# Optimization experiments

Hardware: AMD Instinct MI355X
Metric: run time of the kernel (lower is better)

Reference implementation:

```python
import jax, jax.numpy as jnp
import numpy as np

N, E, D, L, G, C = 20000, 320000, 512, 6, 64, 10
EPS = 1e-5


def setup_inputs() -> dict:
    key = jax.random.key(0)
    ks = jax.random.split(key, 8)
    s = 0.05  # small init scale to keep activations sane across 6 layers
    x = jax.random.normal(ks[0], (N, D), jnp.float32)
    edge_index = jax.random.randint(ks[1], (2, E), 0, N, jnp.int32)
    batch = jnp.sort(jax.random.randint(ks[2], (N,), 0, G, jnp.int32))
    W_rel = jax.random.normal(ks[3], (L, D, D), jnp.float32) * s
    b_rel = jnp.zeros((L, D), jnp.float32)
    W_root = jax.random.normal(ks[4], (L, D, D), jnp.float32) * s
    gamma = jnp.ones((L, D), jnp.float32)
    beta = jnp.zeros((L, D), jnp.float32)
    lin_w = jax.random.normal(ks[5], (D, C), jnp.float32) * s
    lin_b = jnp.zeros((C,), jnp.float32)
    return {"x": x, "edge_index": edge_index, "batch": batch,
            "W_rel": W_rel, "b_rel": b_rel, "W_root": W_root,
            "gamma": gamma, "beta": beta, "lin_w": lin_w, "lin_b": lin_b}


def reference(x, edge_index, batch, W_rel, b_rel, W_root, gamma, beta, lin_w, lin_b):
    # PyG GraphConv (aggr='add'): out = segment_sum(x[src] -> dst) @ W_rel + b_rel + x @ W_root
    src, dst = edge_index[0], edge_index[1]
    n = x.shape[0]
    for l in range(W_rel.shape[0]):  # 6 structurally identical layers
        agg = jax.ops.segment_sum(x[src], dst, num_segments=n)  # [N, D]
        h = agg @ W_rel[l] + b_rel[l] + x @ W_root[l]
        # BatchNorm1d in training mode: biased batch statistics over nodes
        mu = jnp.mean(h, axis=0)
        var = jnp.mean(jnp.square(h - mu), axis=0)
        x = jax.nn.relu((h - mu) * jax.lax.rsqrt(var + EPS) * gamma[l] + beta[l])
    # global_mean_pool over per-node graph ids
    sums = jax.ops.segment_sum(x, batch, num_segments=G)              # [G, D]
    counts = jax.ops.segment_sum(jnp.ones((n,), x.dtype), batch, num_segments=G)
    pooled = sums / jnp.maximum(counts, 1.0)[:, None]
    return pooled @ lin_w + lin_b  # [G, C]
```

## Files before the change

kernel.cpp:

```cpp
#include <hip/hip_runtime.h>


typedef unsigned short u16;
typedef unsigned int u32;
typedef __attribute__((ext_vector_type(8))) short bf16x8;
typedef __attribute__((ext_vector_type(4))) float f32x4;

#define DFEAT 512
#define KDIM 1024
#define NLAYER 6
#define NGRAPH 64
#define NCLS 10
#define BN_EPS 1e-5f

__device__ __forceinline__ float bf_lo(u32 u) { union { u32 i; float f; } v; v.i = u << 16; return v.f; }
__device__ __forceinline__ float bf_hi(u32 u) { union { u32 i; float f; } v; v.i = u & 0xFFFF0000u; return v.f; }
__device__ __forceinline__ u16 f2bf(float f) {
  union { float f; u32 i; } v; v.f = f;
  u32 r = v.i + 0x7FFFu + ((v.i >> 16) & 1u);
  return (u16)(r >> 16);
}
__device__ __forceinline__ u32 pack2(float lo, float hi) {
  return (u32)f2bf(lo) | ((u32)f2bf(hi) << 16);
}

__device__ __forceinline__ void gload_lds16(const u16* g, u16* lds_base) {
  __builtin_amdgcn_global_load_lds(
      (const __attribute__((address_space(1))) u32*)g,
      (__attribute__((address_space(3))) u32*)lds_base, 16, 0, 0);
}

__global__ void hist_kernel(const int* __restrict__ ei, int* __restrict__ counts, int E) {
  int e = blockIdx.x * 256 + threadIdx.x;
  if (e < E) atomicAdd(&counts[ei[E + e]], 1);
}

__global__ __launch_bounds__(1024) void scan_kernel(const int* __restrict__ counts,
                                                    int* __restrict__ row_ptr, int n) {
  __shared__ int buf[1024];
  int tid = threadIdx.x;
  int carry = 0;
  for (int base = 0; base < n; base += 1024) {
    int i = base + tid;
    int v = (i < n) ? counts[i] : 0;
    buf[tid] = v;
    __syncthreads();
    int x = v;
    for (int off = 1; off < 1024; off <<= 1) {
      int t = (tid >= off) ? buf[tid - off] : 0;
      __syncthreads();
      x += t;
      buf[tid] = x;
      __syncthreads();
    }
    if (i < n) row_ptr[i] = carry + x - v;
    int tot = buf[1023];
    __syncthreads();
    carry += tot;
  }
  if (tid == 0) row_ptr[n] = carry;
}

__global__ void scatter_kernel(const int* __restrict__ ei, int* __restrict__ cursor,
                               int* __restrict__ csr_src, int E) {
  int e = blockIdx.x * 256 + threadIdx.x;
  if (e < E) {
    int d = ei[E + e];
    int pos = atomicAdd(&cursor[d], 1);
    csr_src[pos] = ei[e];
  }
}

__global__ void wconv_kernel(const float* __restrict__ Wrel, const float* __restrict__ Wroot,
                             u16* __restrict__ Wt) {
  int idx = blockIdx.x * 256 + threadIdx.x;
  int k = idx & 1023;
  int n = (idx >> 10) & 511;
  int l = idx >> 19;
  float v = (k < DFEAT) ? Wrel[((size_t)l * DFEAT + k) * DFEAT + n]
                        : Wroot[((size_t)l * DFEAT + (k - DFEAT)) * DFEAT + n];
  Wt[idx] = f2bf(v);
}

__global__ void xconv_kernel(const float* __restrict__ x, u16* __restrict__ A, int M) {
  int idx = blockIdx.x * 256 + threadIdx.x;
  int row = idx >> 7;
  int c4 = (idx & 127) * 4;
  if (row >= M) return;
  float4 v = *(const float4*)&x[(size_t)row * DFEAT + c4];
  uint2 o; o.x = pack2(v.x, v.y); o.y = pack2(v.z, v.w);
  *(uint2*)&A[(size_t)row * KDIM + DFEAT + c4] = o;
}

__device__ __forceinline__ void add8(uint4 v, float* a) {
  a[0] += bf_lo(v.x); a[1] += bf_hi(v.x);
  a[2] += bf_lo(v.y); a[3] += bf_hi(v.y);
  a[4] += bf_lo(v.z); a[5] += bf_hi(v.z);
  a[6] += bf_lo(v.w); a[7] += bf_hi(v.w);
}

__global__ __launch_bounds__(256) void gather_kernel(u16* __restrict__ A,
                                                     const int* __restrict__ row_ptr,
                                                     const int* __restrict__ csr_src, int n) {
  int b = blockIdx.x;
  int slice = b & 7;
  int grp = b >> 3;
  int wid = threadIdx.x >> 6, lane = threadIdx.x & 63;
  int dsub = lane >> 3, fl = lane & 7;
  int dst = grp * 32 + wid * 8 + dsub;
  if (dst >= n) return;
  int cc = slice * 64 + fl * 8;
  const u16* Sx = A + DFEAT;
  int beg = row_ptr[dst], end = row_ptr[dst + 1];
  float a[8] = {};
  int e = beg;
  for (; e + 3 < end; e += 4) {
    int s0 = csr_src[e], s1 = csr_src[e + 1], s2 = csr_src[e + 2], s3 = csr_src[e + 3];
    uint4 v0 = *(const uint4*)&Sx[(size_t)s0 * KDIM + cc];
    uint4 v1 = *(const uint4*)&Sx[(size_t)s1 * KDIM + cc];
    uint4 v2 = *(const uint4*)&Sx[(size_t)s2 * KDIM + cc];
    uint4 v3 = *(const uint4*)&Sx[(size_t)s3 * KDIM + cc];
    add8(v0, a); add8(v1, a); add8(v2, a); add8(v3, a);
  }
  for (; e < end; ++e) {
    int s = csr_src[e];
    uint4 v = *(const uint4*)&Sx[(size_t)s * KDIM + cc];
    add8(v, a);
  }
  uint4 o;
  o.x = pack2(a[0], a[1]); o.y = pack2(a[2], a[3]);
  o.z = pack2(a[4], a[5]); o.w = pack2(a[6], a[7]);
  *(uint4*)&A[(size_t)dst * KDIM + cc] = o;
}

#define BM 128
#define BN 128
#define BK 64
__global__ __launch_bounds__(256, 2) void gemm_kernel(const u16* __restrict__ A,
                                                      const u16* __restrict__ Bt,
                                                      const float* __restrict__ bias,
                                                      u16* __restrict__ Hb,
                                                      float* __restrict__ sums, int M) {
  const int lin = blockIdx.x;
  const int bx = ((lin >> 5) << 3) + (lin & 7);
  const int by = (lin >> 3) & 3;
  const int m0 = bx * BM;
  if (m0 >= M) return;
  const int n0 = by * BN;

  __shared__ u16 As[BM * BK];
  __shared__ u16 Bs[BN * BK];
  __shared__ float sred[2 * BN];
  const int tid = threadIdx.x;
  const int wid = tid >> 6, lane = tid & 63;
  const int wm = wid >> 1, wn = wid & 1;
  const int l16 = lane & 15, quad = lane >> 4;

  if (tid < 2 * BN) sred[tid] = 0.f;

  const int dr = lane >> 3;
  const int gcol = ((lane & 7) ^ dr) * 8;
  int arow[4], brow[4];
#pragma unroll
  for (int t = 0; t < 4; t++) {
    int r = wid * 32 + t * 8 + dr;
    int ar = m0 + r; if (ar >= M) ar = M - 1;
    arow[t] = ar;
    brow[t] = n0 + r;
  }

  f32x4 acc[4][4] = {};

  for (int k0 = 0; k0 < KDIM; k0 += BK) {
    __syncthreads();
#pragma unroll
    for (int t = 0; t < 4; t++)
      gload_lds16(&A[(size_t)arow[t] * KDIM + k0 + gcol], &As[(wid * 32 + t * 8) * BK]);
#pragma unroll
    for (int t = 0; t < 4; t++)
      gload_lds16(&Bt[(size_t)brow[t] * KDIM + k0 + gcol], &Bs[(wid * 32 + t * 8) * BK]);
    __syncthreads();
    bf16x8 af[2][4], bfr[2][4];
#pragma unroll
    for (int h = 0; h < 2; h++) {
      int slot = ((h * 4 + quad) ^ (l16 & 7)) * 8;
#pragma unroll
      for (int i = 0; i < 4; i++) {
        af[h][i]  = *(const bf16x8*)&As[(wm * 64 + i * 16 + l16) * BK + slot];
        bfr[h][i] = *(const bf16x8*)&Bs[(wn * 64 + i * 16 + l16) * BK + slot];
      }
    }
#pragma unroll
    for (int h = 0; h < 2; h++)
#pragma unroll
      for (int i = 0; i < 4; i++)
#pragma unroll
        for (int j = 0; j < 4; j++)
          acc[i][j] = __builtin_amdgcn_mfma_f32_16x16x32_bf16(af[h][i], bfr[h][j], acc[i][j], 0, 0, 0);
  }

#pragma unroll
  for (int j = 0; j < 4; j++) {
    int col = n0 + wn * 64 + j * 16 + l16;
    float bv = bias[col];
    float s = 0.f, s2 = 0.f;
#pragma unroll
    for (int i = 0; i < 4; i++) {
      int rbase = m0 + wm * 64 + i * 16 + quad * 4;
#pragma unroll
      for (int r = 0; r < 4; r++) {
        int row = rbase + r;
        if (row < M) {
          float v = acc[i][j][r] + bv;
          Hb[(size_t)row * DFEAT + col] = f2bf(v);
          s += v; s2 += v * v;
        }
      }
    }
    s  += __shfl_xor(s, 16);  s  += __shfl_xor(s, 32);
    s2 += __shfl_xor(s2, 16); s2 += __shfl_xor(s2, 32);
    if (quad == 0) {
      int cl = wn * 64 + j * 16 + l16;
      atomicAdd(&sred[cl], s);
      atomicAdd(&sred[BN + cl], s2);
    }
  }
  __syncthreads();
  if (tid < BN) {
    atomicAdd(&sums[n0 + tid], sred[tid]);
    atomicAdd(&sums[DFEAT + n0 + tid], sred[BN + tid]);
  }
}

__global__ void norm_kernel(const u16* __restrict__ Hb, const float* __restrict__ sums,
                            const float* __restrict__ gamma, const float* __restrict__ beta,
                            u16* __restrict__ A, int M, float invN) {
  int idx = blockIdx.x * 256 + threadIdx.x;
  int row = idx >> 7;
  int c4 = (idx & 127) * 4;
  if (row >= M) return;
  float sc[4], sh[4];
#pragma unroll
  for (int j = 0; j < 4; j++) {
    int c = c4 + j;
    float mu = sums[c] * invN;
    float var = sums[DFEAT + c] * invN - mu * mu;
    float s = gamma[c] * rsqrtf(var + BN_EPS);
    sc[j] = s;
    sh[j] = beta[c] - mu * s;
  }
  uint2 h = *(const uint2*)&Hb[(size_t)row * DFEAT + c4];
  float x0 = fmaxf(bf_lo(h.x) * sc[0] + sh[0], 0.f);
  float x1 = fmaxf(bf_hi(h.x) * sc[1] + sh[1], 0.f);
  float x2 = fmaxf(bf_lo(h.y) * sc[2] + sh[2], 0.f);
  float x3 = fmaxf(bf_hi(h.y) * sc[3] + sh[3], 0.f);
  uint2 o; o.x = pack2(x0, x1); o.y = pack2(x2, x3);
  *(uint2*)&A[(size_t)row * KDIM + DFEAT + c4] = o;
}

__device__ __forceinline__ int lower_bound_dev(const int* a, int n, int v) {
  int lo = 0, hi = n;
  while (lo < hi) { int mid = (lo + hi) >> 1; if (a[mid] < v) lo = mid + 1; else hi = mid; }
  return lo;
}

__global__ __launch_bounds__(1024) void pool_kernel(const u16* __restrict__ Hb,
                                                    const float* __restrict__ sums,
                                                    const float* __restrict__ gamma,
                                                    const float* __restrict__ beta,
                                                    const int* __restrict__ batch,
                                                    float* __restrict__ pooled, int n, float invN) {
  __shared__ float red[DFEAT];
  int g = blockIdx.x;
  int tid = threadIdx.x;
  if (tid < DFEAT) red[tid] = 0.f;
  int lo = lower_bound_dev(batch, n, g);
  int hi = lower_bound_dev(batch, n, g + 1);
  int rowOff = tid >> 6, lane = tid & 63;
  int c0 = lane * 8;
  float sc[8], sh[8];
#pragma unroll
  for (int j = 0; j < 8; j++) {
    int c = c0 + j;
    float mu = sums[c] * invN;
    float var = sums[DFEAT + c] * invN - mu * mu;
    float s = gamma[c] * rsqrtf(var + BN_EPS);
    sc[j] = s;
    sh[j] = beta[c] - mu * s;
  }
  float a[8] = {};
  for (int r = lo + rowOff; r < hi; r += 16) {
    uint4 v = *(const uint4*)&Hb[(size_t)r * DFEAT + c0];
    float e0 = bf_lo(v.x), e1 = bf_hi(v.x), e2 = bf_lo(v.y), e3 = bf_hi(v.y);
    float e4 = bf_lo(v.z), e5 = bf_hi(v.z), e6 = bf_lo(v.w), e7 = bf_hi(v.w);
    a[0] += fmaxf(e0 * sc[0] + sh[0], 0.f); a[1] += fmaxf(e1 * sc[1] + sh[1], 0.f);
    a[2] += fmaxf(e2 * sc[2] + sh[2], 0.f); a[3] += fmaxf(e3 * sc[3] + sh[3], 0.f);
    a[4] += fmaxf(e4 * sc[4] + sh[4], 0.f); a[5] += fmaxf(e5 * sc[5] + sh[5], 0.f);
    a[6] += fmaxf(e6 * sc[6] + sh[6], 0.f); a[7] += fmaxf(e7 * sc[7] + sh[7], 0.f);
  }
  __syncthreads();
#pragma unroll
  for (int j = 0; j < 8; j++) atomicAdd(&red[c0 + j], a[j]);
  __syncthreads();
  if (tid < DFEAT) pooled[g * DFEAT + tid] = red[tid] / fmaxf((float)(hi - lo), 1.0f);
}

__global__ __launch_bounds__(64) void final_kernel(const float* __restrict__ pooled,
                                                   const float* __restrict__ lin_w,
                                                   const float* __restrict__ lin_b,
                                                   float* __restrict__ out) {
  int g = blockIdx.x;
  int lane = threadIdx.x;
  float acc[NCLS] = {};
  float4 p0 = *(const float4*)&pooled[g * DFEAT + lane * 8];
  float4 p1 = *(const float4*)&pooled[g * DFEAT + lane * 8 + 4];
  float pv[8] = {p0.x, p0.y, p0.z, p0.w, p1.x, p1.y, p1.z, p1.w};
#pragma unroll
  for (int j = 0; j < 8; j++) {
    int k = lane * 8 + j;
#pragma unroll
    for (int c = 0; c < NCLS; c++) acc[c] += pv[j] * lin_w[k * NCLS + c];
  }
#pragma unroll
  for (int off = 32; off > 0; off >>= 1)
#pragma unroll
    for (int c = 0; c < NCLS; c++) acc[c] += __shfl_down(acc[c], off);
  if (lane == 0)
#pragma unroll
    for (int c = 0; c < NCLS; c++) out[g * NCLS + c] = acc[c] + lin_b[c];
}

extern "C" void kernel_launch(void* const* d_in, const int* in_sizes, int n_in,
                              void* d_out, int out_size, void* d_ws, size_t ws_size,
                              hipStream_t stream) {
  const float* x      = (const float*)d_in[0];
  const int*   ei     = (const int*)d_in[1];
  const int*   batch  = (const int*)d_in[2];
  const float* W_rel  = (const float*)d_in[3];
  const float* b_rel  = (const float*)d_in[4];
  const float* W_root = (const float*)d_in[5];
  const float* gamma  = (const float*)d_in[6];
  const float* beta   = (const float*)d_in[7];
  const float* lin_w  = (const float*)d_in[8];
  const float* lin_b  = (const float*)d_in[9];
  float* out = (float*)d_out;

  const int N = in_sizes[0] / DFEAT;
  const int E = in_sizes[1] / 2;

  char* p = (char*)d_ws;
  u16*   A       = (u16*)p;    p += (size_t)N * KDIM * 2;
  u16*   Hb      = (u16*)p;    p += (size_t)N * DFEAT * 2;
  u16*   Wt      = (u16*)p;    p += (size_t)NLAYER * DFEAT * KDIM * 2;
  int*   row_ptr = (int*)p;    p += ((size_t)(N + 1) * 4 + 15) / 16 * 16;
  int*   cursor  = (int*)p;    p += (size_t)N * 4;
  int*   csr_src = (int*)p;    p += (size_t)E * 4;
  float* sums    = (float*)p;  p += (size_t)NLAYER * 2 * DFEAT * 4;
  float* pooled  = (float*)p;  p += (size_t)NGRAPH * DFEAT * 4;

  hipMemsetAsync(cursor, 0, (size_t)N * 4, stream);
  hipMemsetAsync(sums, 0, (size_t)NLAYER * 2 * DFEAT * 4, stream);

  hist_kernel<<<(E + 255) / 256, 256, 0, stream>>>(ei, cursor, E);
  scan_kernel<<<1, 1024, 0, stream>>>(cursor, row_ptr, N);
  hipMemcpyAsync(cursor, row_ptr, (size_t)N * 4, hipMemcpyDeviceToDevice, stream);
  scatter_kernel<<<(E + 255) / 256, 256, 0, stream>>>(ei, cursor, csr_src, E);

  wconv_kernel<<<(NLAYER * DFEAT * KDIM) / 256, 256, 0, stream>>>(W_rel, W_root, Wt);
  xconv_kernel<<<(N * 128 + 255) / 256, 256, 0, stream>>>(x, A, N);

  const int ngrp = (N + 31) / 32;
  const int gather_grid = ngrp * 8;
  const int gemm_rows = (N + BM - 1) / BM;
  const int gemm_grid = ((gemm_rows + 7) / 8) * 8 * 4;

  for (int l = 0; l < NLAYER; ++l) {
    float* sums_l = sums + (size_t)l * 2 * DFEAT;
    gather_kernel<<<gather_grid, 256, 0, stream>>>(A, row_ptr, csr_src, N);
    gemm_kernel<<<gemm_grid, 256, 0, stream>>>(A, Wt + (size_t)l * DFEAT * KDIM,
                                               b_rel + (size_t)l * DFEAT, Hb, sums_l, N);
    if (l < NLAYER - 1)
      norm_kernel<<<(N * 128 + 255) / 256, 256, 0, stream>>>(
          Hb, sums_l, gamma + (size_t)l * DFEAT, beta + (size_t)l * DFEAT, A, N, 1.0f / (float)N);
  }

  pool_kernel<<<NGRAPH, 1024, 0, stream>>>(Hb, sums + (size_t)(NLAYER - 1) * 2 * DFEAT,
                                           gamma + (size_t)(NLAYER - 1) * DFEAT,
                                           beta + (size_t)(NLAYER - 1) * DFEAT,
                                           batch, pooled, N, 1.0f / (float)N);
  final_kernel<<<NGRAPH, 64, 0, stream>>>(pooled, lin_w, lin_b, out);
}
```

Measured before the change: 653.9 us.

## Fuse BatchNorm+ReLU into neighbor gather and stage GEMM output through LDS

Drops the separate norm kernel. The next layer's gather now reads the raw bf16 GEMM output Hb, applies BatchNorm scale/shift and ReLU per gathered neighbor, and also writes the normalized self row into the root half of A. The GEMM epilogue writes its tile into shared memory first and then does coalesced 16-byte row stores to Hb, where before it did scattered 2-byte stores. Fusing saves one full read/write pass per layer. In exchange, the gather recomputes the affine+ReLU for each edge, and the GEMM epilogue gains an extra sync and a larger shared buffer.

```diff
diff --git a/kernel.cpp b/kernel.cpp
--- a/kernel.cpp
+++ b/kernel.cpp
@@ -92,14 +92,12 @@
   *(uint2*)&A[(size_t)row * KDIM + DFEAT + c4] = o;
 }
 
-__device__ __forceinline__ void add8(uint4 v, float* a) {
-  a[0] += bf_lo(v.x); a[1] += bf_hi(v.x);
-  a[2] += bf_lo(v.y); a[3] += bf_hi(v.y);
-  a[4] += bf_lo(v.z); a[5] += bf_hi(v.z);
-  a[6] += bf_lo(v.w); a[7] += bf_hi(v.w);
-}
-
 __global__ __launch_bounds__(256) void gather_kernel(u16* __restrict__ A,
+                                                     const u16* __restrict__ S, int sstride,
+                                                     const float* __restrict__ sums,
+                                                     const float* __restrict__ gamma,
+                                                     const float* __restrict__ beta,
+                                                     float invN,
                                                      const int* __restrict__ row_ptr,
                                                      const int* __restrict__ csr_src, int n) {
   int b = blockIdx.x;
@@ -110,32 +108,71 @@
   int dst = grp * 32 + wid * 8 + dsub;
   if (dst >= n) return;
   int cc = slice * 64 + fl * 8;
-  const u16* Sx = A + DFEAT;
+  const bool aff = (sums != nullptr);
+  float sc[8], sh[8];
+#pragma unroll
+  for (int j = 0; j < 8; j++) {
+    if (aff) {
+      int c = cc + j;
+      float mu = sums[c] * invN;
+      float var = sums[DFEAT + c] * invN - mu * mu;
+      float s = gamma[c] * rsqrtf(var + BN_EPS);
+      sc[j] = s;
+      sh[j] = beta[c] - mu * s;
+    } else { sc[j] = 1.f; sh[j] = 0.f; }
+  }
+
+#define AFF8(v, a)                                                          \
+  {                                                                         \
+    float e0 = bf_lo(v.x), e1 = bf_hi(v.x), e2 = bf_lo(v.y), e3 = bf_hi(v.y); \
+    float e4 = bf_lo(v.z), e5 = bf_hi(v.z), e6 = bf_lo(v.w), e7 = bf_hi(v.w); \
+    if (aff) {                                                              \
+      a[0] += fmaxf(e0 * sc[0] + sh[0], 0.f); a[1] += fmaxf(e1 * sc[1] + sh[1], 0.f); \
+      a[2] += fmaxf(e2 * sc[2] + sh[2], 0.f); a[3] += fmaxf(e3 * sc[3] + sh[3], 0.f); \
+      a[4] += fmaxf(e4 * sc[4] + sh[4], 0.f); a[5] += fmaxf(e5 * sc[5] + sh[5], 0.f); \
+      a[6] += fmaxf(e6 * sc[6] + sh[6], 0.f); a[7] += fmaxf(e7 * sc[7] + sh[7], 0.f); \
+    } else {                                                                \
+      a[0] += e0; a[1] += e1; a[2] += e2; a[3] += e3;                       \
+      a[4] += e4; a[5] += e5; a[6] += e6; a[7] += e7;                       \
+    }                                                                       \
+  }
+
   int beg = row_ptr[dst], end = row_ptr[dst + 1];
   float a[8] = {};
   int e = beg;
   for (; e + 3 < end; e += 4) {
     int s0 = csr_src[e], s1 = csr_src[e + 1], s2 = csr_src[e + 2], s3 = csr_src[e + 3];
-    uint4 v0 = *(const uint4*)&Sx[(size_t)s0 * KDIM + cc];
-    uint4 v1 = *(const uint4*)&Sx[(size_t)s1 * KDIM + cc];
-    uint4 v2 = *(const uint4*)&Sx[(size_t)s2 * KDIM + cc];
-    uint4 v3 = *(const uint4*)&Sx[(size_t)s3 * KDIM + cc];
-    add8(v0, a); add8(v1, a); add8(v2, a); add8(v3, a);
+    uint4 v0 = *(const uint4*)&S[(size_t)s0 * sstride + cc];
+    uint4 v1 = *(const uint4*)&S[(size_t)s1 * sstride + cc];
+    uint4 v2 = *(const uint4*)&S[(size_t)s2 * sstride + cc];
+    uint4 v3 = *(const uint4*)&S[(size_t)s3 * sstride + cc];
+    AFF8(v0, a); AFF8(v1, a); AFF8(v2, a); AFF8(v3, a);
   }
   for (; e < end; ++e) {
     int s = csr_src[e];
-    uint4 v = *(const uint4*)&Sx[(size_t)s * KDIM + cc];
-    add8(v, a);
+    uint4 v = *(const uint4*)&S[(size_t)s * sstride + cc];
+    AFF8(v, a);
   }
   uint4 o;
   o.x = pack2(a[0], a[1]); o.y = pack2(a[2], a[3]);
   o.z = pack2(a[4], a[5]); o.w = pack2(a[6], a[7]);
   *(uint4*)&A[(size_t)dst * KDIM + cc] = o;
+
+  if (aff) {
+    uint4 vd = *(const uint4*)&S[(size_t)dst * sstride + cc];
+    float xd[8] = {};
+    AFF8(vd, xd);
+    uint4 ox; ox.x = pack2(xd[0], xd[1]); ox.y = pack2(xd[2], xd[3]);
+    ox.z = pack2(xd[4], xd[5]); ox.w = pack2(xd[6], xd[7]);
+    *(uint4*)&A[(size_t)dst * KDIM + DFEAT + cc] = ox;
+  }
+#undef AFF8
 }
 
 #define BM 128
 #define BN 128
 #define BK 64
+#define CSTR 132
 __global__ __launch_bounds__(256, 2) void gemm_kernel(const u16* __restrict__ A,
                                                       const u16* __restrict__ Bt,
                                                       const float* __restrict__ bias,
@@ -148,9 +185,10 @@
   if (m0 >= M) return;
   const int n0 = by * BN;
 
-  __shared__ u16 As[BM * BK];
-  __shared__ u16 Bs[BN * BK];
+  __shared__ u16 smem[BM * CSTR];
   __shared__ float sred[2 * BN];
+  u16* As = smem;
+  u16* Bs = smem + BM * BK;
   const int tid = threadIdx.x;
   const int wid = tid >> 6, lane = tid & 63;
   const int wm = wid >> 1, wn = wid & 1;
@@ -199,63 +237,48 @@
           acc[i][j] = __builtin_amdgcn_mfma_f32_16x16x32_bf16(af[h][i], bfr[h][j], acc[i][j], 0, 0, 0);
   }
 
+  __syncthreads();
+
 #pragma unroll
   for (int j = 0; j < 4; j++) {
-    int col = n0 + wn * 64 + j * 16 + l16;
-    float bv = bias[col];
+    int colt = wn * 64 + j * 16 + l16;
+    float bv = bias[n0 + colt];
     float s = 0.f, s2 = 0.f;
 #pragma unroll
     for (int i = 0; i < 4; i++) {
-      int rbase = m0 + wm * 64 + i * 16 + quad * 4;
+      int rbase = wm * 64 + i * 16 + quad * 4;
 #pragma unroll
       for (int r = 0; r < 4; r++) {
-        int row = rbase + r;
-        if (row < M) {
-          float v = acc[i][j][r] + bv;
-          Hb[(size_t)row * DFEAT + col] = f2bf(v);
-          s += v; s2 += v * v;
-        }
+        int rowt = rbase + r;
+        float v = acc[i][j][r] + bv;
+        smem[rowt * CSTR + colt] = f2bf(v);
+        if (m0 + rowt < M) { s += v; s2 += v * v; }
       }
     }
     s  += __shfl_xor(s, 16);  s  += __shfl_xor(s, 32);
     s2 += __shfl_xor(s2, 16); s2 += __shfl_xor(s2, 32);
     if (quad == 0) {
-      int cl = wn * 64 + j * 16 + l16;
-      atomicAdd(&sred[cl], s);
-      atomicAdd(&sred[BN + cl], s2);
+      atomicAdd(&sred[colt], s);
+      atomicAdd(&sred[BN + colt], s2);
     }
   }
   __syncthreads();
+
+  const int rsub = tid >> 4;
+  const int c8 = (tid & 15) * 8;
+#pragma unroll
+  for (int it = 0; it < 8; it++) {
+    int rowt = it * 16 + rsub;
+    int grow = m0 + rowt;
+    if (grow < M) {
+      uint4 v = *(const uint4*)&smem[rowt * CSTR + c8];
+      *(uint4*)&Hb[(size_t)grow * DFEAT + n0 + c8] = v;
+    }
+  }
   if (tid < BN) {
     atomicAdd(&sums[n0 + tid], sred[tid]);
     atomicAdd(&sums[DFEAT + n0 + tid], sred[BN + tid]);
   }
-}
-
-__global__ void norm_kernel(const u16* __restrict__ Hb, const float* __restrict__ sums,
-                            const float* __restrict__ gamma, const float* __restrict__ beta,
-                            u16* __restrict__ A, int M, float invN) {
-  int idx = blockIdx.x * 256 + threadIdx.x;
-  int row = idx >> 7;
-  int c4 = (idx & 127) * 4;
-  if (row >= M) return;
-  float sc[4], sh[4];
-#pragma unroll
-  for (int j = 0; j < 4; j++) {
-    int c = c4 + j;
-    float mu = sums[c] * invN;
-    float var = sums[DFEAT + c] * invN - mu * mu;
-    float s = gamma[c] * rsqrtf(var + BN_EPS);
-    sc[j] = s;
-    sh[j] = beta[c] - mu * s;
-  }
-  uint2 h = *(const uint2*)&Hb[(size_t)row * DFEAT + c4];
-  float x0 = fmaxf(bf_lo(h.x) * sc[0] + sh[0], 0.f);
-  float x1 = fmaxf(bf_hi(h.x) * sc[1] + sh[1], 0.f);
-  float x2 = fmaxf(bf_lo(h.y) * sc[2] + sh[2], 0.f);
-  float x3 = fmaxf(bf_hi(h.y) * sc[3] + sh[3], 0.f);
-  uint2 o; o.x = pack2(x0, x1); o.y = pack2(x2, x3);
-  *(uint2*)&A[(size_t)row * KDIM + DFEAT + c4] = o;
 }
 
 __device__ __forceinline__ int lower_bound_dev(const int* a, int n, int v) {
@@ -358,6 +381,8 @@
   float* sums    = (float*)p;  p += (size_t)NLAYER * 2 * DFEAT * 4;
   float* pooled  = (float*)p;  p += (size_t)NGRAPH * DFEAT * 4;
 
+  const float invN = 1.0f / (float)N;
+
   hipMemsetAsync(cursor, 0, (size_t)N * 4, stream);
   hipMemsetAsync(sums, 0, (size_t)NLAYER * 2 * DFEAT * 4, stream);
 
@@ -376,17 +401,23 @@
 
   for (int l = 0; l < NLAYER; ++l) {
     float* sums_l = sums + (size_t)l * 2 * DFEAT;
-    gather_kernel<<<gather_grid, 256, 0, stream>>>(A, row_ptr, csr_src, N);
+    if (l == 0)
+      gather_kernel<<<gather_grid, 256, 0, stream>>>(A, A + DFEAT, KDIM, nullptr,
+                                                     nullptr, nullptr, invN,
+                                                     row_ptr, csr_src, N);
+    else
+      gather_kernel<<<gather_grid, 256, 0, stream>>>(A, Hb, DFEAT,
+                                                     sums + (size_t)(l - 1) * 2 * DFEAT,
+                                                     gamma + (size_t)(l - 1) * DFEAT,
+                                                     beta + (size_t)(l - 1) * DFEAT, invN,
+                                                     row_ptr, csr_src, N);
     gemm_kernel<<<gemm_grid, 256, 0, stream>>>(A, Wt + (size_t)l * DFEAT * KDIM,
                                                b_rel + (size_t)l * DFEAT, Hb, sums_l, N);
-    if (l < NLAYER - 1)
-      norm_kernel<<<(N * 128 + 255) / 256, 256, 0, stream>>>(
-          Hb, sums_l, gamma + (size_t)l * DFEAT, beta + (size_t)l * DFEAT, A, N, 1.0f / (float)N);
   }
 
   pool_kernel<<<NGRAPH, 1024, 0, stream>>>(Hb, sums + (size_t)(NLAYER - 1) * 2 * DFEAT,
                                            gamma + (size_t)(NLAYER - 1) * DFEAT,
                                            beta + (size_t)(NLAYER - 1) * DFEAT,
-                                           batch, pooled, N, 1.0f / (float)N);
+                                           batch, pooled, N, invN);
   final_kernel<<<NGRAPH, 64, 0, stream>>>(pooled, lin_w, lin_b, out);
 }
```

New measurement: 761.8 us. +16.5%, slower.
